# Kernel optimization log

Measured on AMD Instinct MI355X. Metric: run time of the kernel, lower is better.

## Reference

```python
import jax, jax.numpy as jnp
import numpy as np

N_NODES = 100000
N_EDGES = 1600000
HEADS = 4
HID = 32
NEG_SLOPE = 0.2
EPS = 1e-16


def _gat_layer(x, w, a_src, a_dst, b, src, dst, n_nodes, concat):
    # x: [N, F_in], w: [H*C, F_in], a_src/a_dst: [H, C]
    H, C = a_src.shape
    h = (x @ w.T).reshape(-1, H, C)                      # [N, H, C]
    alpha_src = jnp.einsum('nhc,hc->nh', h, a_src)       # [N, H]
    alpha_dst = jnp.einsum('nhc,hc->nh', h, a_dst)       # [N, H]
    e = alpha_src[src] + alpha_dst[dst]                  # [E, H]
    e = jax.nn.leaky_relu(e, NEG_SLOPE)
    # segment softmax over incoming edges of each dst node
    m = jax.ops.segment_max(e, dst, num_segments=n_nodes)   # [N, H]
    ex = jnp.exp(e - m[dst])
    denom = jax.ops.segment_sum(ex, dst, num_segments=n_nodes)  # [N, H]
    alpha = ex / (denom[dst] + EPS)                      # [E, H]
    msg = alpha[:, :, None] * h[src]                     # [E, H, C]
    out = jax.ops.segment_sum(msg, dst, num_segments=n_nodes)  # [N, H, C]
    if concat:
        out = out.reshape(n_nodes, H * C)
    else:
        out = out.mean(axis=1)
    return out + b


def setup_inputs() -> dict:
    key = jax.random.key(0)
    ks = jax.random.split(key, 16)
    x = jax.random.normal(ks[0], (N_NODES, 3), dtype=jnp.float32)
    edge_index = jax.random.randint(ks[1], (2, N_EDGES), 0, N_NODES, dtype=jnp.int64 if jax.config.read('jax_enable_x64') else jnp.int32)
    s = 0.1
    return {
        'x': x,
        'edge_index': edge_index,
        'w1': jax.random.normal(ks[2], (HEADS * HID, 3)) * s,
        'att_src1': jax.random.normal(ks[3], (HEADS, HID)) * s,
        'att_dst1': jax.random.normal(ks[4], (HEADS, HID)) * s,
        'b1': jax.random.normal(ks[5], (HEADS * HID,)) * s,
        'w2': jax.random.normal(ks[6], (HID, HEADS * HID)) * s,
        'att_src2': jax.random.normal(ks[7], (1, HID)) * s,
        'att_dst2': jax.random.normal(ks[8], (1, HID)) * s,
        'b2': jax.random.normal(ks[9], (HID,)) * s,
        'mlp_w1': jax.random.normal(ks[10], (HID, 2 * HID)) * s,
        'mlp_b1': jax.random.normal(ks[11], (HID,)) * s,
        'mlp_w2': jax.random.normal(ks[12], (1, HID)) * s,
        'mlp_b2': jax.random.normal(ks[13], (1,)) * s,
    }


def reference(x, edge_index, w1, att_src1, att_dst1, b1, w2, att_src2, att_dst2, b2,
              mlp_w1, mlp_b1, mlp_w2, mlp_b2):
    src, dst = edge_index[0], edge_index[1]
    n = x.shape[0]
    # dropout layers are identity in eval mode
    h = _gat_layer(x, w1, att_src1, att_dst1, b1, src, dst, n, concat=True)   # [N, H*C]
    h = jax.nn.elu(h)
    h = _gat_layer(h, w2, att_src2, att_dst2, b2, src, dst, n, concat=False)  # [N, C]
    ef = jnp.concatenate([h[src], h[dst]], axis=-1)                            # [E, 2C]
    ef = jax.nn.relu(ef @ mlp_w1.T + mlp_b1)
    flows = (ef @ mlp_w2.T + mlp_b2).squeeze(-1)                               # [E]
    return jax.nn.relu(flows)
```

## Files before the change

kernel.cpp:

```cpp
#include <hip/hip_runtime.h>
#include <hip/hip_fp16.h>
#include <math.h>

#define N_NODES 100000
#define N_EDGES 1600000
#define NEG_SLOPE 0.2f
#define EPS 1e-16f

#define NBUCK 196
#define CHUNK 4096
#define BLKB 391

__device__ __forceinline__ float lrelu(float v) { return v > 0.f ? v : NEG_SLOPE * v; }

__device__ __forceinline__ float4 ld4h(const __half* p) {
    uint2 r = *(const uint2*)p;
    __half2 h0 = *reinterpret_cast<const __half2*>(&r.x);
    __half2 h1 = *reinterpret_cast<const __half2*>(&r.y);
    float2 f0 = __half22float2(h0), f1 = __half22float2(h1);
    return make_float4(f0.x, f0.y, f1.x, f1.y);
}

__device__ __forceinline__ void ld8h(const __half* p, float* f) {
    uint4 r = *(const uint4*)p;
    __half2 h0 = *reinterpret_cast<const __half2*>(&r.x);
    __half2 h1 = *reinterpret_cast<const __half2*>(&r.y);
    __half2 h2 = *reinterpret_cast<const __half2*>(&r.z);
    __half2 h3 = *reinterpret_cast<const __half2*>(&r.w);
    float2 f0 = __half22float2(h0), f1 = __half22float2(h1);
    float2 f2 = __half22float2(h2), f3 = __half22float2(h3);
    f[0] = f0.x; f[1] = f0.y; f[2] = f1.x; f[3] = f1.y;
    f[4] = f2.x; f[5] = f2.y; f[6] = f3.x; f[7] = f3.y;
}

__global__ void kA_hist(const int* __restrict__ ei, int* __restrict__ bh) {
    __shared__ int hist[NBUCK];
    int tid = threadIdx.x, b = blockIdx.x;
    if (tid < NBUCK) hist[tid] = 0;
    __syncthreads();
    int base = b * CHUNK;
    #pragma unroll
    for (int i = 0; i < CHUNK / 256; i++) {
        int e = base + i * 256 + tid;
        if (e < N_EDGES) {
            int dst = ei[N_EDGES + e];
            atomicAdd(&hist[dst >> 9], 1);
        }
    }
    __syncthreads();
    if (tid < NBUCK) bh[b * NBUCK + tid] = hist[tid];
}

__global__ void kS1(int* __restrict__ bh, int* __restrict__ bucketStart) {
    __shared__ int tsum[256];
    int k = blockIdx.x, t = threadIdx.x;
    int j0 = 2 * t, j1 = 2 * t + 1;
    int v0 = (j0 < BLKB) ? bh[j0 * NBUCK + k] : 0;
    int v1 = (j1 < BLKB) ? bh[j1 * NBUCK + k] : 0;
    int s = v0 + v1;
    tsum[t] = s;
    __syncthreads();
    for (int off = 1; off < 256; off <<= 1) {
        int tv = (t >= off) ? tsum[t - off] : 0;
        __syncthreads();
        tsum[t] += tv;
        __syncthreads();
    }
    int excl = tsum[t] - s;
    if (j0 < BLKB) bh[j0 * NBUCK + k] = excl;
    if (j1 < BLKB) bh[j1 * NBUCK + k] = excl + v0;
    if (t == 255) bucketStart[k] = tsum[255];
}

__global__ void kS2(int* __restrict__ bucketStart) {
    __shared__ int tmp[256];
    int t = threadIdx.x;
    int v = (t < NBUCK) ? bucketStart[t] : 0;
    tmp[t] = v;
    __syncthreads();
    for (int off = 1; off < 256; off <<= 1) {
        int tv = (t >= off) ? tmp[t - off] : 0;
        __syncthreads();
        tmp[t] += tv;
        __syncthreads();
    }
    if (t < NBUCK) bucketStart[t] = tmp[t] - v;
    if (t == NBUCK - 1) bucketStart[NBUCK] = tmp[t];
}

__global__ void kB_bin(const int* __restrict__ ei, const int* __restrict__ bh,
                       const int* __restrict__ bucketStart, int* __restrict__ binned) {
    __shared__ int cur[NBUCK];
    int tid = threadIdx.x, b = blockIdx.x;
    if (tid < NBUCK) cur[tid] = bucketStart[tid] + bh[b * NBUCK + tid];
    __syncthreads();
    int base = b * CHUNK;
    #pragma unroll
    for (int i = 0; i < CHUNK / 256; i++) {
        int e = base + i * 256 + tid;
        if (e < N_EDGES) {
            int src = ei[e], dst = ei[N_EDGES + e];
            int pos = atomicAdd(&cur[dst >> 9], 1);
            binned[pos] = src | ((dst & 511) << 17);
        }
    }
}

__global__ void kC_sort(const int* __restrict__ bucketStart, const int* __restrict__ binned,
                        int* __restrict__ deg, int* __restrict__ rowptr,
                        int* __restrict__ csr_src) {
    __shared__ int cnt[512];
    __shared__ int pfx[512];
    __shared__ int bsum[256];
    int t = threadIdx.x, k = blockIdx.x;
    int s0 = bucketStart[k], s1 = bucketStart[k + 1];
    cnt[t] = 0; cnt[t + 256] = 0;
    __syncthreads();
    for (int i = s0 + t; i < s1; i += 256)
        atomicAdd(&cnt[binned[i] >> 17], 1);
    __syncthreads();
    int a0 = cnt[2 * t], a1 = cnt[2 * t + 1];
    int s = a0 + a1;
    bsum[t] = s;
    __syncthreads();
    for (int off = 1; off < 256; off <<= 1) {
        int tv = (t >= off) ? bsum[t - off] : 0;
        __syncthreads();
        bsum[t] += tv;
        __syncthreads();
    }
    int excl = bsum[t] - s;
    pfx[2 * t] = excl;
    pfx[2 * t + 1] = excl + a0;
    int nb0 = k << 9;
    int n0 = nb0 + 2 * t, n1 = nb0 + 2 * t + 1;
    if (n0 < N_NODES) { deg[n0] = a0; rowptr[n0] = s0 + excl; }
    if (n1 < N_NODES) { deg[n1] = a1; rowptr[n1] = s0 + excl + a0; }
    __syncthreads();
    for (int i = s0 + t; i < s1; i += 256) {
        int pkd = binned[i];
        int pos = s0 + atomicAdd(&pfx[pkd >> 17], 1);
        csr_src[pos] = pkd & 0x1FFFF;
    }
}

__global__ void k_q(const float* __restrict__ w1, const float* __restrict__ as1,
                    const float* __restrict__ ad1, float* __restrict__ qv) {
    int t = threadIdx.x;
    if (t >= 24) return;
    int c = t % 3, h = (t / 3) % 4, side = t / 12;
    const float* att = side ? ad1 : as1;
    float acc = 0.f;
    for (int cc = 0; cc < 32; cc++)
        acc += att[h * 32 + cc] * w1[(h * 32 + cc) * 3 + c];
    qv[t] = acc;
}

__global__ void k_node1(const float* __restrict__ x, const float* __restrict__ qv,
                        float* __restrict__ a1d, float* __restrict__ p1) {
    int n = blockIdx.x * blockDim.x + threadIdx.x;
    if (n >= N_NODES) return;
    float x0 = x[n * 3], x1 = x[n * 3 + 1], x2 = x[n * 3 + 2];
    float4 s, d;
    s.x = x0 * qv[0]  + x1 * qv[1]  + x2 * qv[2];
    s.y = x0 * qv[3]  + x1 * qv[4]  + x2 * qv[5];
    s.z = x0 * qv[6]  + x1 * qv[7]  + x2 * qv[8];
    s.w = x0 * qv[9]  + x1 * qv[10] + x2 * qv[11];
    d.x = x0 * qv[12] + x1 * qv[13] + x2 * qv[14];
    d.y = x0 * qv[15] + x1 * qv[16] + x2 * qv[17];
    d.z = x0 * qv[18] + x1 * qv[19] + x2 * qv[20];
    d.w = x0 * qv[21] + x1 * qv[22] + x2 * qv[23];
    ((float4*)a1d)[n] = d;
    ((float4*)p1)[n * 2]     = s;
    float4 xx; xx.x = x0; xx.y = x1; xx.z = x2; xx.w = 1.f;
    ((float4*)p1)[n * 2 + 1] = xx;
}

#define G1_BLOCKS ((N_NODES + 63) / 64)
__global__ void k_gat1(const int* __restrict__ rowptr, const int* __restrict__ deg,
                       const int* __restrict__ csr_src,
                       const float* __restrict__ p1, const float* __restrict__ w1,
                       const float* __restrict__ a1d,
                       const float* __restrict__ b1, const float* __restrict__ w2,
                       const float* __restrict__ as2, const float* __restrict__ ad2,
                       __half* __restrict__ h2, float* __restrict__ a2s, float* __restrict__ a2d) {
    __shared__ float sm[64][16];
    __shared__ float f1s[4][128];
    int tid = threadIdx.x;
    int wave = tid >> 6, lane = tid & 63;
    int o = lane & 31, half = lane >> 5;
    int k0 = half * 64;

    int nl = wave * 16 + (lane >> 2);
    int h  = lane & 3;
    int n  = blockIdx.x * 64 + nl;
    if (n < N_NODES) {
        float4 ad4 = ((const float4*)a1d)[n];
        float adv[4] = {ad4.x, ad4.y, ad4.z, ad4.w};
        int beg = rowptr[n], cnt = deg[n];
        float acc[4][4];
        #pragma unroll
        for (int hh = 0; hh < 4; hh++)
            acc[hh][0] = acc[hh][1] = acc[hh][2] = acc[hh][3] = 0.f;
        int t = h;
        for (; t + 4 < cnt; t += 8) {
            int i0 = csr_src[beg + t], i1 = csr_src[beg + t + 4];
            float4 A0 = ((const float4*)p1)[i0 * 2], X0 = ((const float4*)p1)[i0 * 2 + 1];
            float4 A1 = ((const float4*)p1)[i1 * 2], X1 = ((const float4*)p1)[i1 * 2 + 1];
            float a0v[4] = {A0.x, A0.y, A0.z, A0.w};
            float a1v[4] = {A1.x, A1.y, A1.z, A1.w};
            #pragma unroll
            for (int hh = 0; hh < 4; hh++) {
                float e0 = __expf(lrelu(a0v[hh] + adv[hh]));
                float e1 = __expf(lrelu(a1v[hh] + adv[hh]));
                acc[hh][0] += e0 * X0.x + e1 * X1.x;
                acc[hh][1] += e0 * X0.y + e1 * X1.y;
                acc[hh][2] += e0 * X0.z + e1 * X1.z;
                acc[hh][3] += e0 + e1;
            }
        }
        if (t < cnt) {
            int i0 = csr_src[beg + t];
            float4 A0 = ((const float4*)p1)[i0 * 2], X0 = ((const float4*)p1)[i0 * 2 + 1];
            float a0v[4] = {A0.x, A0.y, A0.z, A0.w};
            #pragma unroll
            for (int hh = 0; hh < 4; hh++) {
                float e0 = __expf(lrelu(a0v[hh] + adv[hh]));
                acc[hh][0] += e0 * X0.x;
                acc[hh][1] += e0 * X0.y;
                acc[hh][2] += e0 * X0.z;
                acc[hh][3] += e0;
            }
        }
        #pragma unroll
        for (int hh = 0; hh < 4; hh++) {
            #pragma unroll
            for (int cc = 0; cc < 4; cc++) {
                float vv = acc[hh][cc];
                vv += __shfl_xor(vv, 1);
                vv += __shfl_xor(vv, 2);
                acc[hh][cc] = vv;
            }
        }
        float4 r;
        r.x = h == 0 ? acc[0][0] : h == 1 ? acc[1][0] : h == 2 ? acc[2][0] : acc[3][0];
        r.y = h == 0 ? acc[0][1] : h == 1 ? acc[1][1] : h == 2 ? acc[2][1] : acc[3][1];
        r.z = h == 0 ? acc[0][2] : h == 1 ? acc[1][2] : h == 2 ? acc[2][2] : acc[3][2];
        r.w = h == 0 ? acc[0][3] : h == 1 ? acc[1][3] : h == 2 ? acc[2][3] : acc[3][3];
        *(float4*)&sm[nl][h * 4] = r;
    }

    float w2r[64];
    {
        const float4* wp = (const float4*)(w2 + o * 128 + k0);
        #pragma unroll
        for (int q = 0; q < 16; q++) {
            float4 t = wp[q];
            w2r[q * 4 + 0] = t.x; w2r[q * 4 + 1] = t.y;
            w2r[q * 4 + 2] = t.z; w2r[q * 4 + 3] = t.w;
        }
    }

    int j = lane, j2 = lane + 64;
    int h0 = j >> 5;
    float wa0 = w1[j * 3], wa1 = w1[j * 3 + 1], wa2 = w1[j * 3 + 2];
    float wb0 = w1[j2 * 3], wb1 = w1[j2 * 3 + 1], wb2 = w1[j2 * 3 + 2];
    float b1j = b1[j], b1j2 = b1[j2];
    float as2o = as2[o], ad2o = ad2[o];
    const float* f = f1s[wave];

    #pragma unroll 1
    for (int i = 0; i < 16; i++) {
        int n2 = blockIdx.x * 64 + wave * 16 + i;
        if (n2 >= N_NODES) break;
        const float* S = sm[wave * 16 + i];
        float v0 = (wa0 * S[h0 * 4] + wa1 * S[h0 * 4 + 1] + wa2 * S[h0 * 4 + 2])
                   / (S[h0 * 4 + 3] + EPS) + b1j;
        float v1 = (wb0 * S[(2 + h0) * 4] + wb1 * S[(2 + h0) * 4 + 1] + wb2 * S[(2 + h0) * 4 + 2])
                   / (S[(2 + h0) * 4 + 3] + EPS) + b1j2;
        f1s[wave][j]  = v0 > 0.f ? v0 : expm1f(v0);
        f1s[wave][j2] = v1 > 0.f ? v1 : expm1f(v1);
        float acc = 0.f;
        #pragma unroll
        for (int t = 0; t < 64; t++)
            acc += f[k0 + t] * w2r[t];
        acc += __shfl_down(acc, 32);
        if (half == 0) {
            h2[n2 * 32 + o] = __float2half(acc);
            float ps = acc * as2o, pd = acc * ad2o;
            #pragma unroll
            for (int off = 16; off; off >>= 1) {
                ps += __shfl_xor(ps, off);
                pd += __shfl_xor(pd, off);
            }
            if (o == 0) { a2s[n2] = ps; a2d[n2] = pd; }
        }
    }
}

#define G2_BLOCKS ((N_NODES + 15) / 16)
__global__ void k_gat2(const int* __restrict__ rowptr, const int* __restrict__ deg,
                       const int* __restrict__ csr_src,
                       const __half* __restrict__ h2, const float* __restrict__ a2s,
                       const float* __restrict__ a2d, const float* __restrict__ b2,
                       const float* __restrict__ mw1, const float* __restrict__ mb1,
                       __half* __restrict__ u, __half* __restrict__ v) {
    __shared__ float Ws2[2][32 * 36];
    __shared__ int2  pk[4][64];
    __shared__ float4 hfs[4][4][8];
    int tid = threadIdx.x;
    for (int i = tid; i < 2048; i += 256) {
        int c = i >> 6, col = i & 63;
        Ws2[col >> 5][c * 36 + (col & 31)] = mw1[i];
    }
    __syncthreads();
    int lane = tid & 63, w = tid >> 6;
    int nl = lane >> 4, sl = lane & 15;
    int eg2 = sl >> 2, qq = sl & 3;
    int n = blockIdx.x * 16 + w * 4 + nl;
    float4 b2a = ((const float4*)b2)[qq * 2];
    float4 b2b = ((const float4*)b2)[qq * 2 + 1];

    int beg = 0, cnt = 0;
    float ad = 0.f;
    if (n < N_NODES) { beg = rowptr[n]; cnt = deg[n]; ad = a2d[n]; }

    float acc[8] = {0.f, 0.f, 0.f, 0.f, 0.f, 0.f, 0.f, 0.f};
    float den = 0.f;
    int pkbase = (nl << 4);
    for (int b16 = 0; b16 < cnt; b16 += 16) {
        int li = b16 + sl;
        int idx = (li < cnt) ? csr_src[beg + li] : 0;
        float e = 0.f;
        if (li < cnt) e = __expf(lrelu(a2s[idx] + ad));
        den += e;
        pk[w][pkbase + sl] = make_int2(idx, __float_as_int(e));
        #pragma unroll
        for (int p = 0; p < 4; p++) {
            int2 pe = pk[w][pkbase + p * 4 + eg2];
            float g[8];
            ld8h(h2 + pe.x * 32 + qq * 8, g);
            float ee = __int_as_float(pe.y);
            acc[0] += ee * g[0]; acc[1] += ee * g[1];
            acc[2] += ee * g[2]; acc[3] += ee * g[3];
            acc[4] += ee * g[4]; acc[5] += ee * g[5];
            acc[6] += ee * g[6]; acc[7] += ee * g[7];
        }
    }
    #pragma unroll
    for (int j = 0; j < 8; j++) {
        float vv = acc[j];
        vv += __shfl_xor(vv, 4);
        vv += __shfl_xor(vv, 8);
        acc[j] = vv;
    }
    den += __shfl_xor(den, 1); den += __shfl_xor(den, 2);
    den += __shfl_xor(den, 4); den += __shfl_xor(den, 8);
    float inv = 1.f / (den + EPS);
    if (sl < 4) {
        float4 ha, hb;
        ha.x = acc[0] * inv + b2a.x; ha.y = acc[1] * inv + b2a.y;
        ha.z = acc[2] * inv + b2a.z; ha.w = acc[3] * inv + b2a.w;
        hb.x = acc[4] * inv + b2b.x; hb.y = acc[5] * inv + b2b.y;
        hb.z = acc[6] * inv + b2b.z; hb.w = acc[7] * inv + b2b.w;
        hfs[w][nl][qq * 2]     = ha;
        hfs[w][nl][qq * 2 + 1] = hb;
    }
    if (n < N_NODES) {
        int half_o = sl >> 3, c4 = (sl & 7) * 4;
        __half* outp = half_o ? v : u;
        float r0 = half_o ? 0.f : mb1[c4 + 0];
        float r1 = half_o ? 0.f : mb1[c4 + 1];
        float r2 = half_o ? 0.f : mb1[c4 + 2];
        float r3 = half_o ? 0.f : mb1[c4 + 3];
        const float* Wb = &Ws2[half_o][0];
        #pragma unroll
        for (int q = 0; q < 8; q++) {
            float4 hq = hfs[w][nl][q];
            float4 W0 = *(const float4*)&Wb[(c4 + 0) * 36 + q * 4];
            float4 W1 = *(const float4*)&Wb[(c4 + 1) * 36 + q * 4];
            float4 W2 = *(const float4*)&Wb[(c4 + 2) * 36 + q * 4];
            float4 W3 = *(const float4*)&Wb[(c4 + 3) * 36 + q * 4];
            r0 += W0.x * hq.x + W0.y * hq.y + W0.z * hq.z + W0.w * hq.w;
            r1 += W1.x * hq.x + W1.y * hq.y + W1.z * hq.z + W1.w * hq.w;
            r2 += W2.x * hq.x + W2.y * hq.y + W2.z * hq.z + W2.w * hq.w;
            r3 += W3.x * hq.x + W3.y * hq.y + W3.z * hq.z + W3.w * hq.w;
        }
        __half2 p0, p1;
        p0.x = __float2half(r0); p0.y = __float2half(r1);
        p1.x = __float2half(r2); p1.y = __float2half(r3);
        uint2 st;
        st.x = *reinterpret_cast<unsigned int*>(&p0);
        st.y = *reinterpret_cast<unsigned int*>(&p1);
        *reinterpret_cast<uint2*>(outp + n * 32 + c4) = st;
    }
}

#define MLP_BLOCKS 4096
__global__ void k_mlp(const int* __restrict__ ei, const __half* __restrict__ u,
                      const __half* __restrict__ v, const float* __restrict__ mw2,
                      const float* __restrict__ mb2, float* __restrict__ out) {
    int tid = threadIdx.x;
    int q = tid & 7;
    float4 w2q = ((const float4*)mw2)[q];
    float mb20 = mb2[0];
    int g = blockIdx.x * 32 + (tid >> 3);
    const int stride = MLP_BLOCKS * 32 * 4;
    for (int e = g * 4; e < N_EDGES; e += stride) {
        int eb = e;
        int e1 = (eb + 1 < N_EDGES) ? eb + 1 : eb;
        int e2 = (eb + 2 < N_EDGES) ? eb + 2 : eb;
        int e3 = (eb + 3 < N_EDGES) ? eb + 3 : eb;
        int sa = ei[eb], da = ei[N_EDGES + eb];
        int sb = ei[e1], db = ei[N_EDGES + e1];
        int sc = ei[e2], dc = ei[N_EDGES + e2];
        int sd = ei[e3], dd = ei[N_EDGES + e3];
        float4 ua = ld4h(u + sa * 32 + q * 4);
        float4 va = ld4h(v + da * 32 + q * 4);
        float4 ub = ld4h(u + sb * 32 + q * 4);
        float4 vb = ld4h(v + db * 32 + q * 4);
        float4 uc = ld4h(u + sc * 32 + q * 4);
        float4 vc = ld4h(v + dc * 32 + q * 4);
        float4 ud = ld4h(u + sd * 32 + q * 4);
        float4 vd = ld4h(v + dd * 32 + q * 4);
        float s0 = fmaxf(ua.x + va.x, 0.f) * w2q.x + fmaxf(ua.y + va.y, 0.f) * w2q.y
                 + fmaxf(ua.z + va.z, 0.f) * w2q.z + fmaxf(ua.w + va.w, 0.f) * w2q.w;
        float s1 = fmaxf(ub.x + vb.x, 0.f) * w2q.x + fmaxf(ub.y + vb.y, 0.f) * w2q.y
                 + fmaxf(ub.z + vb.z, 0.f) * w2q.z + fmaxf(ub.w + vb.w, 0.f) * w2q.w;
        float s2 = fmaxf(uc.x + vc.x, 0.f) * w2q.x + fmaxf(uc.y + vc.y, 0.f) * w2q.y
                 + fmaxf(uc.z + vc.z, 0.f) * w2q.z + fmaxf(uc.w + vc.w, 0.f) * w2q.w;
        float s3 = fmaxf(ud.x + vd.x, 0.f) * w2q.x + fmaxf(ud.y + vd.y, 0.f) * w2q.y
                 + fmaxf(ud.z + vd.z, 0.f) * w2q.z + fmaxf(ud.w + vd.w, 0.f) * w2q.w;
        s0 += __shfl_xor(s0, 1, 8); s0 += __shfl_xor(s0, 2, 8); s0 += __shfl_xor(s0, 4, 8);
        s1 += __shfl_xor(s1, 1, 8); s1 += __shfl_xor(s1, 2, 8); s1 += __shfl_xor(s1, 4, 8);
        s2 += __shfl_xor(s2, 1, 8); s2 += __shfl_xor(s2, 2, 8); s2 += __shfl_xor(s2, 4, 8);
        s3 += __shfl_xor(s3, 1, 8); s3 += __shfl_xor(s3, 2, 8); s3 += __shfl_xor(s3, 4, 8);
        if (q == 0) {
            out[eb] = fmaxf(s0 + mb20, 0.f);
            if (eb + 1 < N_EDGES) out[eb + 1] = fmaxf(s1 + mb20, 0.f);
            if (eb + 2 < N_EDGES) out[eb + 2] = fmaxf(s2 + mb20, 0.f);
            if (eb + 3 < N_EDGES) out[eb + 3] = fmaxf(s3 + mb20, 0.f);
        }
    }
}

extern "C" void kernel_launch(void* const* d_in, const int* in_sizes, int n_in,
                              void* d_out, int out_size, void* d_ws, size_t ws_size,
                              hipStream_t stream) {
    const float* x    = (const float*)d_in[0];
    const int*   ei   = (const int*)d_in[1];
    const float* w1   = (const float*)d_in[2];
    const float* as1  = (const float*)d_in[3];
    const float* ad1  = (const float*)d_in[4];
    const float* b1   = (const float*)d_in[5];
    const float* w2   = (const float*)d_in[6];
    const float* as2  = (const float*)d_in[7];
    const float* ad2  = (const float*)d_in[8];
    const float* b2   = (const float*)d_in[9];
    const float* mw1  = (const float*)d_in[10];
    const float* mb1  = (const float*)d_in[11];
    const float* mw2  = (const float*)d_in[12];
    const float* mb2  = (const float*)d_in[13];
    float* out = (float*)d_out;

    const int N = N_NODES;
    char* base   = (char*)d_ws;
    int* deg     = (int*)(base);
    int* rowptr  = (int*)(base + 400000);
    int* bstart  = (int*)(base + 800000);
    int* bh      = (int*)(base + 1200000);
    int* csr_src = (int*)(base + 1602048);
    float* p1    = (float*)(base + 8002048);
    float* a1d   = (float*)(base + 11202048);
    __half* h2   = (__half*)(base + 12802048);
    int* binned  = (int*)(base + 19202048);
    float* a2s   = (float*)(base + 25602048);
    float* a2d   = (float*)(base + 26002048);
    __half* u    = (__half*)(base + 26402048);
    __half* v    = (__half*)(base + 32802048);
    float* qv    = (float*)(base + 39202048);

    const int nb = (N + 255) / 256;

    kA_hist<<<BLKB, 256, 0, stream>>>(ei, bh);
    kS1<<<NBUCK, 256, 0, stream>>>(bh, bstart);
    kS2<<<1, 256, 0, stream>>>(bstart);
    kB_bin<<<BLKB, 256, 0, stream>>>(ei, bh, bstart, binned);
    kC_sort<<<NBUCK, 256, 0, stream>>>(bstart, binned, deg, rowptr, csr_src);

    k_q<<<1, 32, 0, stream>>>(w1, as1, ad1, qv);
    k_node1<<<nb, 256, 0, stream>>>(x, qv, a1d, p1);

    k_gat1<<<G1_BLOCKS, 256, 0, stream>>>(rowptr, deg, csr_src, p1, w1, a1d,
                                          b1, w2, as2, ad2, h2, a2s, a2d);

    k_gat2<<<G2_BLOCKS, 256, 0, stream>>>(rowptr, deg, csr_src, h2, a2s, a2d, b2,
                                          mw1, mb1, u, v);

    k_mlp<<<MLP_BLOCKS, 256, 0, stream>>>(ei, u, v, mw2, mb2, out);
}
```

Before: 284.5 us.

## Compute layer-2 projection in k_gat1 with fp16 MFMA instead of scalar FMAs

The per-node 32x128 matrix-vector product in k_gat1 was done with scalar FMAs over 64-element register slices plus a shuffle reduction. It is now batched over 16 nodes per wave into a half-precision LDS tile and computed with mfma_f32_16x16x32_f16, with W2 preconverted to fp16 fragments in registers. The attention dot products are reduced across the MFMA output layout with shuffles. This also swaps expm1f for __expf-1 and rounds the ELU activations to fp16, which lowers precision.

Result: faster. 260.6 us (-8.4%).

```diff
diff --git a/kernel.cpp b/kernel.cpp
--- a/kernel.cpp
+++ b/kernel.cpp
@@ -10,6 +10,9 @@
 #define NBUCK 196
 #define CHUNK 4096
 #define BLKB 391
+
+typedef _Float16 f16x8 __attribute__((ext_vector_type(8)));
+typedef float f32x4 __attribute__((ext_vector_type(4)));
 
 __device__ __forceinline__ float lrelu(float v) { return v > 0.f ? v : NEG_SLOPE * v; }
 
@@ -185,11 +188,9 @@
                        const float* __restrict__ as2, const float* __restrict__ ad2,
                        __half* __restrict__ h2, float* __restrict__ a2s, float* __restrict__ a2d) {
     __shared__ float sm[64][16];
-    __shared__ float f1s[4][128];
+    __shared__ __align__(16) __half F1h[4][16][136];
     int tid = threadIdx.x;
     int wave = tid >> 6, lane = tid & 63;
-    int o = lane & 31, half = lane >> 5;
-    int k0 = half * 64;
 
     int nl = wave * 16 + (lane >> 2);
     int h  = lane & 3;
@@ -250,14 +251,23 @@
         *(float4*)&sm[nl][h * 4] = r;
     }
 
-    float w2r[64];
+    f16x8 Bf[2][4];
     {
-        const float4* wp = (const float4*)(w2 + o * 128 + k0);
-        #pragma unroll
-        for (int q = 0; q < 16; q++) {
-            float4 t = wp[q];
-            w2r[q * 4 + 0] = t.x; w2r[q * 4 + 1] = t.y;
-            w2r[q * 4 + 2] = t.z; w2r[q * 4 + 3] = t.w;
+        int bn = lane & 15, bg = lane >> 4;
+        #pragma unroll
+        for (int tile = 0; tile < 2; tile++) {
+            const float* wrow = w2 + (tile * 16 + bn) * 128 + bg * 8;
+            #pragma unroll
+            for (int ks = 0; ks < 4; ks++) {
+                const float4* wp = (const float4*)(wrow + ks * 32);
+                float4 u0 = wp[0], u1 = wp[1];
+                f16x8 bf;
+                bf[0] = (_Float16)u0.x; bf[1] = (_Float16)u0.y;
+                bf[2] = (_Float16)u0.z; bf[3] = (_Float16)u0.w;
+                bf[4] = (_Float16)u1.x; bf[5] = (_Float16)u1.y;
+                bf[6] = (_Float16)u1.z; bf[7] = (_Float16)u1.w;
+                Bf[tile][ks] = bf;
+            }
         }
     }
 
@@ -266,8 +276,6 @@
     float wa0 = w1[j * 3], wa1 = w1[j * 3 + 1], wa2 = w1[j * 3 + 2];
     float wb0 = w1[j2 * 3], wb1 = w1[j2 * 3 + 1], wb2 = w1[j2 * 3 + 2];
     float b1j = b1[j], b1j2 = b1[j2];
-    float as2o = as2[o], ad2o = ad2[o];
-    const float* f = f1s[wave];
 
     #pragma unroll 1
     for (int i = 0; i < 16; i++) {
@@ -278,22 +286,43 @@
                    / (S[h0 * 4 + 3] + EPS) + b1j;
         float v1 = (wb0 * S[(2 + h0) * 4] + wb1 * S[(2 + h0) * 4 + 1] + wb2 * S[(2 + h0) * 4 + 2])
                    / (S[(2 + h0) * 4 + 3] + EPS) + b1j2;
-        f1s[wave][j]  = v0 > 0.f ? v0 : expm1f(v0);
-        f1s[wave][j2] = v1 > 0.f ? v1 : expm1f(v1);
-        float acc = 0.f;
-        #pragma unroll
-        for (int t = 0; t < 64; t++)
-            acc += f[k0 + t] * w2r[t];
-        acc += __shfl_down(acc, 32);
-        if (half == 0) {
-            h2[n2 * 32 + o] = __float2half(acc);
-            float ps = acc * as2o, pd = acc * ad2o;
-            #pragma unroll
-            for (int off = 16; off; off >>= 1) {
-                ps += __shfl_xor(ps, off);
-                pd += __shfl_xor(pd, off);
+        float e0 = v0 > 0.f ? v0 : __expf(v0) - 1.f;
+        float e1 = v1 > 0.f ? v1 : __expf(v1) - 1.f;
+        F1h[wave][i][j]  = __float2half(e0);
+        F1h[wave][i][j2] = __float2half(e1);
+    }
+
+    f32x4 d0 = {0.f, 0.f, 0.f, 0.f}, d1 = {0.f, 0.f, 0.f, 0.f};
+    {
+        int am = lane & 15, ag = lane >> 4;
+        const __half* Arow = &F1h[wave][am][0];
+        #pragma unroll
+        for (int ks = 0; ks < 4; ks++) {
+            f16x8 af = *(const f16x8*)&Arow[ks * 32 + ag * 8];
+            d0 = __builtin_amdgcn_mfma_f32_16x16x32_f16(af, Bf[0][ks], d0, 0, 0, 0);
+            d1 = __builtin_amdgcn_mfma_f32_16x16x32_f16(af, Bf[1][ks], d1, 0, 0, 0);
+        }
+    }
+
+    {
+        int ch = lane & 15, rg = lane >> 4;
+        float as2a = as2[ch], as2b = as2[ch + 16];
+        float ad2a = ad2[ch], ad2b = ad2[ch + 16];
+        #pragma unroll
+        for (int r = 0; r < 4; r++) {
+            int n2 = blockIdx.x * 64 + wave * 16 + rg * 4 + r;
+            float va = d0[r], vb = d1[r];
+            if (n2 < N_NODES) {
+                h2[n2 * 32 + ch]      = __float2half(va);
+                h2[n2 * 32 + ch + 16] = __float2half(vb);
             }
-            if (o == 0) { a2s[n2] = ps; a2d[n2] = pd; }
+            float ps = va * as2a + vb * as2b;
+            float pd = va * ad2a + vb * ad2b;
+            ps += __shfl_xor(ps, 1); ps += __shfl_xor(ps, 2);
+            ps += __shfl_xor(ps, 4); ps += __shfl_xor(ps, 8);
+            pd += __shfl_xor(pd, 1); pd += __shfl_xor(pd, 2);
+            pd += __shfl_xor(pd, 4); pd += __shfl_xor(pd, 8);
+            if (ch == 0 && n2 < N_NODES) { a2s[n2] = ps; a2d[n2] = pd; }
         }
     }
 }
```
